# Performance work log

Measured on AMD Instinct MI355X. Metric: run time of the kernel, lower is better.

## Reference

```python
import jax, jax.numpy as jnp
import numpy as np

EPS = 1e-08


def setup_inputs() -> dict:
    key = jax.random.key(0)
    k1, k2 = jax.random.split(key)
    B, N, D2 = 8, 2048, 2048  # N = extended_len, D2 = 2*D
    x = jax.random.normal(k1, (B, N, D2), dtype=jnp.float32)
    # xavier_normal_ for a square [N, N] matrix: std = sqrt(2/(N+N)) = sqrt(1/N)
    spatial_proj = jax.random.normal(k2, (N, N), dtype=jnp.float32) * np.sqrt(1.0 / N)
    return {"x": x, "spatial_proj": spatial_proj}


def reference(x, spatial_proj):
    # split channels: x0 drives attention, x1 gates the output
    x0, x1 = jnp.split(x, 2, axis=-1)  # each [B, N, D]
    # cosine similarity of x0 with itself
    norm = jnp.sqrt(jnp.sum(x0 * x0, axis=-1, keepdims=True) + EPS)
    xn = x0 / norm  # [B, N, D]
    cosim = jnp.einsum('bnd,bmd->bnm', xn, xn)  # [B, N, N]
    # learned causal mask (lower-triangular), no softmax
    mask = jnp.tril(spatial_proj)  # [N, N]
    attn = mask[None, :, :] * cosim  # [B, N, N]
    ctx = jnp.einsum('bnm,bmd->bnd', attn, x0)  # [B, N, D]
    return ctx * x1
```

## Files before the change

### kernel.cpp

```cpp
#include <hip/hip_runtime.h>
#include <cstdint>

#define NB 8
#define NN 2048
#define DD 1024
#define DD2 2048
#define BK 64

typedef short short8 __attribute__((ext_vector_type(8)));
typedef float floatx4 __attribute__((ext_vector_type(4)));

__device__ __forceinline__ unsigned short f2bf(float f) {
    unsigned int u = __float_as_uint(f);
    u += 0x7fffu + ((u >> 16) & 1u);
    return (unsigned short)(u >> 16);
}

__device__ __forceinline__ void async_copy16(const void* g, void* l) {
    __builtin_amdgcn_global_load_lds(
        (__attribute__((address_space(1))) void*)(uintptr_t)g,
        (__attribute__((address_space(3))) void*)(unsigned int)(uintptr_t)l,
        16, 0, 0);
}

__global__ __launch_bounds__(256) void k_norm(const float* __restrict__ x,
                                              unsigned short* __restrict__ xn) {
    int row  = blockIdx.x * 4 + (threadIdx.x >> 6);
    int lane = threadIdx.x & 63;
    const float* xr = x + (size_t)row * DD2;
    float4 v[4];
    float s = 0.f;
#pragma unroll
    for (int i = 0; i < 4; i++) {
        v[i] = ((const float4*)xr)[lane + i * 64];
        s += v[i].x * v[i].x + v[i].y * v[i].y + v[i].z * v[i].z + v[i].w * v[i].w;
    }
#pragma unroll
    for (int off = 32; off >= 1; off >>= 1) s += __shfl_xor(s, off, 64);
    float inv = 1.0f / sqrtf(s + 1e-8f);
    unsigned short* xnr = xn + (size_t)row * DD;
#pragma unroll
    for (int i = 0; i < 4; i++) {
        ushort4 o;
        o.x = f2bf(v[i].x * inv);
        o.y = f2bf(v[i].y * inv);
        o.z = f2bf(v[i].z * inv);
        o.w = f2bf(v[i].w * inv);
        ((ushort4*)xnr)[lane + i * 64] = o;
    }
}

__global__ __launch_bounds__(256) void k_transpose(const float* __restrict__ x,
                                                   unsigned short* __restrict__ x0t) {
    __shared__ unsigned short tile[64 * 68];
    int b  = blockIdx.y;
    int t  = blockIdx.x;
    int nt = t >> 4;
    int dt = t & 15;
    int n0 = nt * 64, d0 = dt * 64;
    int tid = threadIdx.x;
    int r  = tid >> 4;
    int c4 = tid & 15;
    const float* xb = x + (size_t)b * NN * DD2;
#pragma unroll
    for (int p = 0; p < 4; p++) {
        int n = p * 16 + r;
        float4 v = *(const float4*)&xb[(size_t)(n0 + n) * DD2 + d0 + c4 * 4];
        tile[(c4 * 4 + 0) * 68 + n] = f2bf(v.x);
        tile[(c4 * 4 + 1) * 68 + n] = f2bf(v.y);
        tile[(c4 * 4 + 2) * 68 + n] = f2bf(v.z);
        tile[(c4 * 4 + 3) * 68 + n] = f2bf(v.w);
    }
    __syncthreads();
    unsigned short* ob = x0t + (size_t)b * DD * NN;
#pragma unroll
    for (int p = 0; p < 4; p++) {
        int d = p * 16 + r;
        ushort4 o;
        o.x = tile[d * 68 + c4 * 4 + 0];
        o.y = tile[d * 68 + c4 * 4 + 1];
        o.z = tile[d * 68 + c4 * 4 + 2];
        o.w = tile[d * 68 + c4 * 4 + 3];
        *(ushort4*)&ob[(size_t)(d0 + d) * NN + n0 + c4 * 4] = o;
    }
}

__device__ __forceinline__ void stage_tile(const unsigned short* gbase, int ld,
                                           unsigned short* lds, int w, int lane) {
    int rgrp = lane >> 3;
    int slot = lane & 7;
    int sw   = slot ^ rgrp;
#pragma unroll
    for (int j = 0; j < 4; j++) {
        int r = j * 32 + w * 8 + rgrp;
        const unsigned short* g = gbase + (size_t)r * ld + sw * 8;
        unsigned short* l = lds + (j * 32 + w * 8) * BK;
        async_copy16((void*)g, (void*)l);
    }
}

__device__ __forceinline__ short8 read_frag(const unsigned short* lds, int row, int g) {
    int slot = g ^ (row & 7);
    return *(const short8*)(lds + row * BK + slot * 8);
}

__device__ __forceinline__ void gemm_core(const unsigned short* __restrict__ Ag, int lda,
                                          const unsigned short* __restrict__ Bg, int ldb,
                                          int kIters,
                                          unsigned short* As, unsigned short* Bs,
                                          floatx4 acc[4][4]) {
    int tid  = threadIdx.x;
    int w    = tid >> 6, lane = tid & 63;
    int wr   = (w >> 1) * 64, wc = (w & 1) * 64;
    int lrow = lane & 15, quad = lane >> 4;
    for (int kt = 0; kt < kIters; kt++) {
        __syncthreads();
        stage_tile(Ag + kt * BK, lda, As, w, lane);
        stage_tile(Bg + kt * BK, ldb, Bs, w, lane);
        __syncthreads();
#pragma unroll
        for (int s = 0; s < 2; s++) {
            short8 af[4], bf[4];
#pragma unroll
            for (int t = 0; t < 4; t++) af[t] = read_frag(As, wr + t * 16 + lrow, s * 4 + quad);
#pragma unroll
            for (int t = 0; t < 4; t++) bf[t] = read_frag(Bs, wc + t * 16 + lrow, s * 4 + quad);
#pragma unroll
            for (int ti = 0; ti < 4; ti++)
#pragma unroll
                for (int tj = 0; tj < 4; tj++)
                    acc[ti][tj] = __builtin_amdgcn_mfma_f32_16x16x32_bf16(
                        af[ti], bf[tj], acc[ti][tj], 0, 0, 0);
        }
    }
}

__global__ __launch_bounds__(256) void k_cosim(const unsigned short* __restrict__ xn,
                                               const float* __restrict__ sp,
                                               unsigned short* __restrict__ attn) {
    __shared__ __attribute__((aligned(16))) unsigned short As[128 * BK];
    __shared__ __attribute__((aligned(16))) unsigned short Bs[128 * BK];
    int b = blockIdx.y;
    int p = blockIdx.x;
    int nt = 0;
    while ((nt + 1) * (nt + 2) / 2 <= p) nt++;
    int mt = p - nt * (nt + 1) / 2;
    int n0 = nt * 128, m0 = mt * 128;
    const unsigned short* xb = xn + (size_t)b * NN * DD;

    floatx4 acc[4][4];
#pragma unroll
    for (int i = 0; i < 4; i++)
#pragma unroll
        for (int j = 0; j < 4; j++) acc[i][j] = (floatx4)0.0f;

    gemm_core(xb + (size_t)n0 * DD, DD, xb + (size_t)m0 * DD, DD, DD / BK, As, Bs, acc);

    int tid = threadIdx.x, w = tid >> 6, lane = tid & 63;
    int wr = (w >> 1) * 64, wc = (w & 1) * 64;
    int col = lane & 15, quad = lane >> 4;
    unsigned short* ab = attn + (size_t)b * NN * NN;
#pragma unroll
    for (int ti = 0; ti < 4; ti++)
#pragma unroll
        for (int tj = 0; tj < 4; tj++)
#pragma unroll
            for (int r = 0; r < 4; r++) {
                int n = n0 + wr + ti * 16 + quad * 4 + r;
                int m = m0 + wc + tj * 16 + col;
                float v = acc[ti][tj][r];
                float s = sp[(size_t)n * NN + m];
                float o = (m <= n) ? s * v : 0.0f;
                ab[(size_t)n * NN + m] = f2bf(o);
            }
}

__global__ __launch_bounds__(256) void k_ctx(const unsigned short* __restrict__ attn,
                                             const unsigned short* __restrict__ x0t,
                                             const float* __restrict__ x,
                                             float* __restrict__ out) {
    __shared__ __attribute__((aligned(16))) unsigned short As[128 * BK];
    __shared__ __attribute__((aligned(16))) unsigned short Bs[128 * BK];
    int b = blockIdx.y;
    int q = blockIdx.x;
    int nt = 15 - (q >> 3);
    int dt = q & 7;
    int n0 = nt * 128, d0 = dt * 128;
    const unsigned short* Ab = attn + (size_t)b * NN * NN + (size_t)n0 * NN;
    const unsigned short* Bb = x0t + (size_t)b * DD * NN + (size_t)d0 * NN;

    floatx4 acc[4][4];
#pragma unroll
    for (int i = 0; i < 4; i++)
#pragma unroll
        for (int j = 0; j < 4; j++) acc[i][j] = (floatx4)0.0f;

    gemm_core(Ab, NN, Bb, NN, (nt + 1) * 2, As, Bs, acc);

    int tid = threadIdx.x, w = tid >> 6, lane = tid & 63;
    int wr = (w >> 1) * 64, wc = (w & 1) * 64;
    int col = lane & 15, quad = lane >> 4;
#pragma unroll
    for (int ti = 0; ti < 4; ti++)
#pragma unroll
        for (int tj = 0; tj < 4; tj++)
#pragma unroll
            for (int r = 0; r < 4; r++) {
                int n = n0 + wr + ti * 16 + quad * 4 + r;
                int d = d0 + wc + tj * 16 + col;
                float x1 = x[((size_t)b * NN + n) * DD2 + DD + d];
                out[((size_t)b * NN + n) * DD + d] = acc[ti][tj][r] * x1;
            }
}

extern "C" void kernel_launch(void* const* d_in, const int* in_sizes, int n_in,
                              void* d_out, int out_size, void* d_ws, size_t ws_size,
                              hipStream_t stream) {
    const float* x  = (const float*)d_in[0];
    const float* sp = (const float*)d_in[1];
    float* out = (float*)d_out;

    unsigned short* xn   = (unsigned short*)d_ws;
    unsigned short* x0t  = xn + (size_t)NB * NN * DD;
    unsigned short* attn = x0t + (size_t)NB * NN * DD;

    hipLaunchKernelGGL(k_norm,      dim3(NB * NN / 4), dim3(256), 0, stream, x, xn);
    hipLaunchKernelGGL(k_transpose, dim3(512, NB),     dim3(256), 0, stream, x, x0t);
    hipLaunchKernelGGL(k_cosim,     dim3(136, NB),     dim3(256), 0, stream, xn, sp, attn);
    hipLaunchKernelGGL(k_ctx,       dim3(128, NB),     dim3(256), 0, stream, attn, x0t, x, out);
}
```

Before: 371.7 us.

## Double-buffer LDS tiles in GEMM core and interleave batches across blocks

Adds a second pair of LDS buffers so the async global-to-LDS copies for the next K tile are issued before the MFMA work on the current tile. A partial vmcnt wait replaces the full wait, so loads can overlap with compute. Both GEMM kernels also move from a 2D grid to a flat grid with the batch index in the low bits, which spreads work from different batches across concurrently running blocks. LDS use per block doubles, which may reduce occupancy, and the hand-written waitcnt count depends on each thread issuing exactly 8 loads per stage.

```diff
diff --git a/kernel.cpp b/kernel.cpp
--- a/kernel.cpp
+++ b/kernel.cpp
@@ -107,24 +107,38 @@
 __device__ __forceinline__ void gemm_core(const unsigned short* __restrict__ Ag, int lda,
                                           const unsigned short* __restrict__ Bg, int ldb,
                                           int kIters,
-                                          unsigned short* As, unsigned short* Bs,
+                                          unsigned short* As0, unsigned short* Bs0,
+                                          unsigned short* As1, unsigned short* Bs1,
                                           floatx4 acc[4][4]) {
     int tid  = threadIdx.x;
     int w    = tid >> 6, lane = tid & 63;
     int wr   = (w >> 1) * 64, wc = (w & 1) * 64;
     int lrow = lane & 15, quad = lane >> 4;
+
+    stage_tile(Ag, lda, As0, w, lane);
+    stage_tile(Bg, ldb, Bs0, w, lane);
+
     for (int kt = 0; kt < kIters; kt++) {
-        __syncthreads();
-        stage_tile(Ag + kt * BK, lda, As, w, lane);
-        stage_tile(Bg + kt * BK, ldb, Bs, w, lane);
-        __syncthreads();
+        unsigned short* Ac = (kt & 1) ? As1 : As0;
+        unsigned short* Bc = (kt & 1) ? Bs1 : Bs0;
+        if (kt + 1 < kIters) {
+            unsigned short* An = (kt & 1) ? As0 : As1;
+            unsigned short* Bn = (kt & 1) ? Bs0 : Bs1;
+            stage_tile(Ag + (size_t)(kt + 1) * BK, lda, An, w, lane);
+            stage_tile(Bg + (size_t)(kt + 1) * BK, ldb, Bn, w, lane);
+            asm volatile("s_waitcnt vmcnt(8)" ::: "memory");
+        } else {
+            asm volatile("s_waitcnt vmcnt(0)" ::: "memory");
+        }
+        __builtin_amdgcn_s_barrier();
+        asm volatile("" ::: "memory");
 #pragma unroll
         for (int s = 0; s < 2; s++) {
             short8 af[4], bf[4];
 #pragma unroll
-            for (int t = 0; t < 4; t++) af[t] = read_frag(As, wr + t * 16 + lrow, s * 4 + quad);
-#pragma unroll
-            for (int t = 0; t < 4; t++) bf[t] = read_frag(Bs, wc + t * 16 + lrow, s * 4 + quad);
+            for (int t = 0; t < 4; t++) af[t] = read_frag(Ac, wr + t * 16 + lrow, s * 4 + quad);
+#pragma unroll
+            for (int t = 0; t < 4; t++) bf[t] = read_frag(Bc, wc + t * 16 + lrow, s * 4 + quad);
 #pragma unroll
             for (int ti = 0; ti < 4; ti++)
 #pragma unroll
@@ -132,16 +146,21 @@
                     acc[ti][tj] = __builtin_amdgcn_mfma_f32_16x16x32_bf16(
                         af[ti], bf[tj], acc[ti][tj], 0, 0, 0);
         }
+        asm volatile("" ::: "memory");
+        __builtin_amdgcn_s_barrier();
     }
 }
 
 __global__ __launch_bounds__(256) void k_cosim(const unsigned short* __restrict__ xn,
                                                const float* __restrict__ sp,
                                                unsigned short* __restrict__ attn) {
-    __shared__ __attribute__((aligned(16))) unsigned short As[128 * BK];
-    __shared__ __attribute__((aligned(16))) unsigned short Bs[128 * BK];
-    int b = blockIdx.y;
-    int p = blockIdx.x;
+    __shared__ __attribute__((aligned(16))) unsigned short As0[128 * BK];
+    __shared__ __attribute__((aligned(16))) unsigned short Bs0[128 * BK];
+    __shared__ __attribute__((aligned(16))) unsigned short As1[128 * BK];
+    __shared__ __attribute__((aligned(16))) unsigned short Bs1[128 * BK];
+    int L = blockIdx.x;
+    int b = L & 7;
+    int p = L >> 3;
     int nt = 0;
     while ((nt + 1) * (nt + 2) / 2 <= p) nt++;
     int mt = p - nt * (nt + 1) / 2;
@@ -154,7 +173,8 @@
 #pragma unroll
         for (int j = 0; j < 4; j++) acc[i][j] = (floatx4)0.0f;
 
-    gemm_core(xb + (size_t)n0 * DD, DD, xb + (size_t)m0 * DD, DD, DD / BK, As, Bs, acc);
+    gemm_core(xb + (size_t)n0 * DD, DD, xb + (size_t)m0 * DD, DD, DD / BK,
+              As0, Bs0, As1, Bs1, acc);
 
     int tid = threadIdx.x, w = tid >> 6, lane = tid & 63;
     int wr = (w >> 1) * 64, wc = (w & 1) * 64;
@@ -179,12 +199,15 @@
                                              const unsigned short* __restrict__ x0t,
                                              const float* __restrict__ x,
                                              float* __restrict__ out) {
-    __shared__ __attribute__((aligned(16))) unsigned short As[128 * BK];
-    __shared__ __attribute__((aligned(16))) unsigned short Bs[128 * BK];
-    int b = blockIdx.y;
-    int q = blockIdx.x;
-    int nt = 15 - (q >> 3);
-    int dt = q & 7;
+    __shared__ __attribute__((aligned(16))) unsigned short As0[128 * BK];
+    __shared__ __attribute__((aligned(16))) unsigned short Bs0[128 * BK];
+    __shared__ __attribute__((aligned(16))) unsigned short As1[128 * BK];
+    __shared__ __attribute__((aligned(16))) unsigned short Bs1[128 * BK];
+    int L = blockIdx.x;
+    int b = L & 7;
+    int j = L >> 3;
+    int nt = 15 - (j >> 3);
+    int dt = j & 7;
     int n0 = nt * 128, d0 = dt * 128;
     const unsigned short* Ab = attn + (size_t)b * NN * NN + (size_t)n0 * NN;
     const unsigned short* Bb = x0t + (size_t)b * DD * NN + (size_t)d0 * NN;
@@ -193,9 +216,9 @@
 #pragma unroll
     for (int i = 0; i < 4; i++)
 #pragma unroll
-        for (int j = 0; j < 4; j++) acc[i][j] = (floatx4)0.0f;
-
-    gemm_core(Ab, NN, Bb, NN, (nt + 1) * 2, As, Bs, acc);
+        for (int jj = 0; jj < 4; jj++) acc[i][jj] = (floatx4)0.0f;
+
+    gemm_core(Ab, NN, Bb, NN, (nt + 1) * 2, As0, Bs0, As1, Bs1, acc);
 
     int tid = threadIdx.x, w = tid >> 6, lane = tid & 63;
     int wr = (w >> 1) * 64, wc = (w & 1) * 64;
@@ -226,6 +249,6 @@
 
     hipLaunchKernelGGL(k_norm,      dim3(NB * NN / 4), dim3(256), 0, stream, x, xn);
     hipLaunchKernelGGL(k_transpose, dim3(512, NB),     dim3(256), 0, stream, x, x0t);
-    hipLaunchKernelGGL(k_cosim,     dim3(136, NB),     dim3(256), 0, stream, xn, sp, attn);
-    hipLaunchKernelGGL(k_ctx,       dim3(128, NB),     dim3(256), 0, stream, attn, x0t, x, out);
-}
+    hipLaunchKernelGGL(k_cosim,     dim3(136 * NB),    dim3(256), 0, stream, xn, sp, attn);
+    hipLaunchKernelGGL(k_ctx,       dim3(128 * NB),    dim3(256), 0, stream, attn, x0t, x, out);
+}
```

After: 328.3 us. 11.7% less time.

## Replace LDS-staged GEMM with direct register fragment loads and balance ctx tiles

Applied to the files above, without the earlier changes.

Drops the LDS staging (global_load_lds plus two barriers per k-step) and loads MFMA fragments straight from global memory into registers, double-buffered across k-steps. k_ctx now pairs a long and a short triangular tile per block for load balance, and both GEMM kernels use a flattened grid with the batch index in the low bits. Without LDS sharing, each wave fetches its own fragments, so global/L2 traffic rises and the loads are short per-lane 16B reads. Register pressure also grows under the launch_bounds(256,2) occupancy hint.

```diff
diff --git a/kernel.cpp b/kernel.cpp
--- a/kernel.cpp
+++ b/kernel.cpp
@@ -5,7 +5,6 @@
 #define NN 2048
 #define DD 1024
 #define DD2 2048
-#define BK 64
 
 typedef short short8 __attribute__((ext_vector_type(8)));
 typedef float floatx4 __attribute__((ext_vector_type(4)));
@@ -14,13 +13,6 @@
     unsigned int u = __float_as_uint(f);
     u += 0x7fffu + ((u >> 16) & 1u);
     return (unsigned short)(u >> 16);
-}
-
-__device__ __forceinline__ void async_copy16(const void* g, void* l) {
-    __builtin_amdgcn_global_load_lds(
-        (__attribute__((address_space(1))) void*)(uintptr_t)g,
-        (__attribute__((address_space(3))) void*)(unsigned int)(uintptr_t)l,
-        16, 0, 0);
 }
 
 __global__ __launch_bounds__(256) void k_norm(const float* __restrict__ x,
@@ -85,63 +77,61 @@
     }
 }
 
-__device__ __forceinline__ void stage_tile(const unsigned short* gbase, int ld,
-                                           unsigned short* lds, int w, int lane) {
-    int rgrp = lane >> 3;
-    int slot = lane & 7;
-    int sw   = slot ^ rgrp;
-#pragma unroll
-    for (int j = 0; j < 4; j++) {
-        int r = j * 32 + w * 8 + rgrp;
-        const unsigned short* g = gbase + (size_t)r * ld + sw * 8;
-        unsigned short* l = lds + (j * 32 + w * 8) * BK;
-        async_copy16((void*)g, (void*)l);
-    }
-}
-
-__device__ __forceinline__ short8 read_frag(const unsigned short* lds, int row, int g) {
-    int slot = g ^ (row & 7);
-    return *(const short8*)(lds + row * BK + slot * 8);
-}
-
-__device__ __forceinline__ void gemm_core(const unsigned short* __restrict__ Ag, int lda,
-                                          const unsigned short* __restrict__ Bg, int ldb,
-                                          int kIters,
-                                          unsigned short* As, unsigned short* Bs,
-                                          floatx4 acc[4][4]) {
+struct Frags { short8 v[4][2]; };
+
+__device__ __forceinline__ void load_frags(Frags& f, const unsigned short* base,
+                                           int ld, int kcol) {
+#pragma unroll
+    for (int t = 0; t < 4; t++)
+#pragma unroll
+        for (int s = 0; s < 2; s++)
+            f.v[t][s] = *(const short8*)(base + (size_t)(t * 16) * ld + kcol + s * 32);
+}
+
+__device__ __forceinline__ void mfma_frags(const Frags& a, const Frags& b,
+                                           floatx4 acc[4][4]) {
+#pragma unroll
+    for (int s = 0; s < 2; s++)
+#pragma unroll
+        for (int ti = 0; ti < 4; ti++)
+#pragma unroll
+            for (int tj = 0; tj < 4; tj++)
+                acc[ti][tj] = __builtin_amdgcn_mfma_f32_16x16x32_bf16(
+                    a.v[ti][s], b.v[tj][s], acc[ti][tj], 0, 0, 0);
+}
+
+__device__ __forceinline__ void gemm_reg(const unsigned short* __restrict__ Ag, int lda,
+                                         const unsigned short* __restrict__ Bg, int ldb,
+                                         int kIters,
+                                         floatx4 acc[4][4]) {
     int tid  = threadIdx.x;
     int w    = tid >> 6, lane = tid & 63;
     int wr   = (w >> 1) * 64, wc = (w & 1) * 64;
     int lrow = lane & 15, quad = lane >> 4;
-    for (int kt = 0; kt < kIters; kt++) {
-        __syncthreads();
-        stage_tile(Ag + kt * BK, lda, As, w, lane);
-        stage_tile(Bg + kt * BK, ldb, Bs, w, lane);
-        __syncthreads();
-#pragma unroll
-        for (int s = 0; s < 2; s++) {
-            short8 af[4], bf[4];
-#pragma unroll
-            for (int t = 0; t < 4; t++) af[t] = read_frag(As, wr + t * 16 + lrow, s * 4 + quad);
-#pragma unroll
-            for (int t = 0; t < 4; t++) bf[t] = read_frag(Bs, wc + t * 16 + lrow, s * 4 + quad);
-#pragma unroll
-            for (int ti = 0; ti < 4; ti++)
-#pragma unroll
-                for (int tj = 0; tj < 4; tj++)
-                    acc[ti][tj] = __builtin_amdgcn_mfma_f32_16x16x32_bf16(
-                        af[ti], bf[tj], acc[ti][tj], 0, 0, 0);
+    const unsigned short* Ab = Ag + (size_t)(wr + lrow) * lda + quad * 8;
+    const unsigned short* Bb = Bg + (size_t)(wc + lrow) * ldb + quad * 8;
+
+    Frags a0, b0, a1, b1;
+    load_frags(a0, Ab, lda, 0);
+    load_frags(b0, Bb, ldb, 0);
+    for (int kt = 0; kt < kIters; kt += 2) {
+        load_frags(a1, Ab, lda, (kt + 1) * 64);
+        load_frags(b1, Bb, ldb, (kt + 1) * 64);
+        mfma_frags(a0, b0, acc);
+        if (kt + 2 < kIters) {
+            load_frags(a0, Ab, lda, (kt + 2) * 64);
+            load_frags(b0, Bb, ldb, (kt + 2) * 64);
         }
-    }
-}
-
-__global__ __launch_bounds__(256) void k_cosim(const unsigned short* __restrict__ xn,
-                                               const float* __restrict__ sp,
-                                               unsigned short* __restrict__ attn) {
-    __shared__ __attribute__((aligned(16))) unsigned short As[128 * BK];
-    __shared__ __attribute__((aligned(16))) unsigned short Bs[128 * BK];
-    int b = blockIdx.y;
-    int p = blockIdx.x;
+        mfma_frags(a1, b1, acc);
+    }
+}
+
+__global__ __launch_bounds__(256, 2) void k_cosim(const unsigned short* __restrict__ xn,
+                                                  const float* __restrict__ sp,
+                                                  unsigned short* __restrict__ attn) {
+    int L = blockIdx.x;
+    int b = L & 7;
+    int p = L >> 3;
     int nt = 0;
     while ((nt + 1) * (nt + 2) / 2 <= p) nt++;
     int mt = p - nt * (nt + 1) / 2;
@@ -154,7 +144,7 @@
 #pragma unroll
         for (int j = 0; j < 4; j++) acc[i][j] = (floatx4)0.0f;
 
-    gemm_core(xb + (size_t)n0 * DD, DD, xb + (size_t)m0 * DD, DD, DD / BK, As, Bs, acc);
+    gemm_reg(xb + (size_t)n0 * DD, DD, xb + (size_t)m0 * DD, DD, DD / 64, acc);
 
     int tid = threadIdx.x, w = tid >> 6, lane = tid & 63;
     int wr = (w >> 1) * 64, wc = (w & 1) * 64;
@@ -175,42 +165,47 @@
             }
 }
 
-__global__ __launch_bounds__(256) void k_ctx(const unsigned short* __restrict__ attn,
-                                             const unsigned short* __restrict__ x0t,
-                                             const float* __restrict__ x,
-                                             float* __restrict__ out) {
-    __shared__ __attribute__((aligned(16))) unsigned short As[128 * BK];
-    __shared__ __attribute__((aligned(16))) unsigned short Bs[128 * BK];
-    int b = blockIdx.y;
-    int q = blockIdx.x;
-    int nt = 15 - (q >> 3);
-    int dt = q & 7;
-    int n0 = nt * 128, d0 = dt * 128;
-    const unsigned short* Ab = attn + (size_t)b * NN * NN + (size_t)n0 * NN;
-    const unsigned short* Bb = x0t + (size_t)b * DD * NN + (size_t)d0 * NN;
-
-    floatx4 acc[4][4];
-#pragma unroll
-    for (int i = 0; i < 4; i++)
-#pragma unroll
-        for (int j = 0; j < 4; j++) acc[i][j] = (floatx4)0.0f;
-
-    gemm_core(Ab, NN, Bb, NN, (nt + 1) * 2, As, Bs, acc);
+__global__ __launch_bounds__(256, 2) void k_ctx(const unsigned short* __restrict__ attn,
+                                                const unsigned short* __restrict__ x0t,
+                                                const float* __restrict__ x,
+                                                float* __restrict__ out) {
+    int L = blockIdx.x;
+    int b = L & 7;
+    int k = L >> 3;
 
     int tid = threadIdx.x, w = tid >> 6, lane = tid & 63;
     int wr = (w >> 1) * 64, wc = (w & 1) * 64;
     int col = lane & 15, quad = lane >> 4;
-#pragma unroll
-    for (int ti = 0; ti < 4; ti++)
-#pragma unroll
-        for (int tj = 0; tj < 4; tj++)
-#pragma unroll
-            for (int r = 0; r < 4; r++) {
-                int n = n0 + wr + ti * 16 + quad * 4 + r;
-                int d = d0 + wc + tj * 16 + col;
-                float x1 = x[((size_t)b * NN + n) * DD2 + DD + d];
-                out[((size_t)b * NN + n) * DD + d] = acc[ti][tj][r] * x1;
-            }
+
+#pragma unroll
+    for (int it = 0; it < 2; it++) {
+        int r0 = (it == 0) ? k : (127 - k);
+        int nt = 15 - (r0 >> 3);
+        int dt = r0 & 7;
+        int n0 = nt * 128, d0 = dt * 128;
+        const unsigned short* Ab = attn + (size_t)b * NN * NN + (size_t)n0 * NN;
+        const unsigned short* Bb = x0t + (size_t)b * DD * NN + (size_t)d0 * NN;
+
+        floatx4 acc[4][4];
+#pragma unroll
+        for (int i = 0; i < 4; i++)
+#pragma unroll
+            for (int jj = 0; jj < 4; jj++) acc[i][jj] = (floatx4)0.0f;
+
+        gemm_reg(Ab, NN, Bb, NN, (nt + 1) * 2, acc);
+
+#pragma unroll
+        for (int ti = 0; ti < 4; ti++)
+#pragma unroll
+            for (int tj = 0; tj < 4; tj++)
+#pragma unroll
+                for (int rr = 0; rr < 4; rr++) {
+                    int n = n0 + wr + ti * 16 + quad * 4 + rr;
+                    int d = d0 + wc + tj * 16 + col;
+                    float x1 = x[((size_t)b * NN + n) * DD2 + DD + d];
+                    out[((size_t)b * NN + n) * DD + d] = acc[ti][tj][rr] * x1;
+                }
+    }
 }
 
 extern "C" void kernel_launch(void* const* d_in, const int* in_sizes, int n_in,
@@ -226,6 +221,6 @@
 
     hipLaunchKernelGGL(k_norm,      dim3(NB * NN / 4), dim3(256), 0, stream, x, xn);
     hipLaunchKernelGGL(k_transpose, dim3(512, NB),     dim3(256), 0, stream, x, x0t);
-    hipLaunchKernelGGL(k_cosim,     dim3(136, NB),     dim3(256), 0, stream, xn, sp, attn);
-    hipLaunchKernelGGL(k_ctx,       dim3(128, NB),     dim3(256), 0, stream, attn, x0t, x, out);
-}
+    hipLaunchKernelGGL(k_cosim,     dim3(136 * NB),    dim3(256), 0, stream, xn, sp, attn);
+    hipLaunchKernelGGL(k_ctx,       dim3(128 * NB),    dim3(256), 0, stream, attn, x0t, x, out);
+}
```

Result: slower. 629.2 us (+69.3%).
